# Kernel optimization log

Measured on AMD Instinct MI355X. Metric: run time of the kernel, lower is better.

## Reference

```python
import jax, jax.numpy as jnp
import numpy as np

ROUTINGS = 3

def _squash_size1(s):
    # Faithful to squash(tensor, dim=-1) applied on a size-1 last dim:
    # squared_norm degenerates to elementwise s**2.
    sq = s * s
    return (sq / (1.0 + sq)) * s / jnp.sqrt(sq + 1e-9)

def setup_inputs() -> dict:
    key = jax.random.key(0)
    k1, k2 = jax.random.split(key)
    B, I, Din = 16, 1152, 16
    N, D = 32, 64
    inputs = jax.random.normal(k1, (B, I, Din), dtype=jnp.float32)
    W = jax.random.normal(k2, (1, N, I, D, Din), dtype=jnp.float32)
    return {"inputs": inputs, "W": W}

def reference(inputs, W):
    # inputs: [B, I, Din]; W: [1, N, I, D, Din]
    # torch: matmul(W, inputs.unsqueeze(1).unsqueeze(4)) -> [B,N,I,D,1]; drop trailing 1.
    x_hat = jnp.einsum('nidk,bik->bnid', W[0], inputs)  # [B, N, I, D]
    b = jnp.zeros_like(x_hat)                            # [B, N, I, D] (quirk: carries D axis)
    outputs = None
    for i in range(ROUTINGS):
        c = jax.nn.softmax(b, axis=2)                    # softmax over input capsules
        s = jnp.sum(c * x_hat, axis=2)                   # [B, N, D]
        outputs = _squash_size1(s)                       # elementwise squash (size-1 dim quirk)
        if i < ROUTINGS - 1:
            # (inputs_hat * outputs).sum(dim=-1) over size-1 dim == elementwise product
            b = b + x_hat * outputs[:, :, None, :]
    return outputs[..., None]                            # [B, N, D, 1] (after squeeze(2))
```

## Files before the change

### kernel.cpp

```cpp
#include <hip/hip_runtime.h>
#include <hip/hip_bf16.h>
#include <math.h>

#define B_   16
#define N_   32
#define I_   1152
#define DIN  16
#define D_   64
#define TI   8
#define IB   (I_/TI)
#define IC   16
#define BND  (B_*N_*D_)

#if __has_builtin(__builtin_amdgcn_exp2f)
#define EXP2(x) __builtin_amdgcn_exp2f(x)
#else
#define EXP2(x) exp2f(x)
#endif

#define LOG2E 1.4426950408889634f

typedef __attribute__((ext_vector_type(8))) short short8v;
typedef __attribute__((ext_vector_type(4))) float f32x4;
typedef __attribute__((ext_vector_type(4))) unsigned int u32x4;
typedef __attribute__((ext_vector_type(2))) unsigned int u32x2;

__device__ __forceinline__ float squash1(float s) {
    float sq = s * s;
    return (sq / (1.0f + sq)) * s * rsqrtf(sq + 1e-9f);
}
__device__ __forceinline__ unsigned short bfh(float v) {
    return __builtin_bit_cast(unsigned short, __float2bfloat16(v));
}
__device__ __forceinline__ float bff(unsigned short u) {
    unsigned int x = ((unsigned int)u) << 16;
    return __builtin_bit_cast(float, x);
}

__global__ __launch_bounds__(256, 4) void k_xhat(const float* __restrict__ inp,
                                                 const float* __restrict__ W,
                                                 unsigned short* __restrict__ xh2,
                                                 float* __restrict__ part) {
    __shared__ __align__(16) unsigned short xs[2048];
    const int bx = blockIdx.x;
    const int n  = bx / IB;
    const int ib = bx % IB;
    const int i0 = ib * TI;
    const int t  = threadIdx.x;
    const int l  = t & 63;
    const int mt = t >> 6;
    const int row = l & 15;
    const int ko  = (l >> 4) & 1;

    {
        const int sb  = t >> 4;
        const int sil = (t >> 1) & 7;
        const int sko = t & 1;
        const float* src = inp + (size_t)sb * (I_ * DIN) + (size_t)(i0 + sil) * DIN + sko * 8;
        f32x4 a0 = *(const f32x4*)src;
        f32x4 a1 = *(const f32x4*)(src + 4);
        u32x4 p;
        p.x = ((unsigned)bfh(a0.y) << 16) | bfh(a0.x);
        p.y = ((unsigned)bfh(a0.w) << 16) | bfh(a0.z);
        p.z = ((unsigned)bfh(a1.y) << 16) | bfh(a1.x);
        p.w = ((unsigned)bfh(a1.w) << 16) | bfh(a1.z);
        int base = (sb * 256 + sil * 32 + sko * 16) ^ ((sb & 7) << 4);
        *(u32x4*)((char*)xs + base) = p;
    }
    __syncthreads();

    const float* wb = W + ((size_t)(n * I_ + i0) * 64 + mt * 16 + row) * 16 + ko * 8;
    f32x4 wv[16];
    #pragma unroll
    for (int i = 0; i < 8; ++i) {
        const f32x4* p = (const f32x4*)(wb + (size_t)i * 1024);
        wv[2 * i] = p[0]; wv[2 * i + 1] = p[1];
    }

    f32x4 acc[TI];
    #pragma unroll
    for (int i = 0; i < TI; ++i) acc[i] = (f32x4){0.f, 0.f, 0.f, 0.f};

    const bool loHalf = (l >= 32);
    #pragma unroll
    for (int i = 0; i < TI; ++i) {
        int xaddr = ((l & 15) * 256 + i * 32 + ko * 16) ^ (((l & 15) & 7) << 4);
        short8v bfrag = *(const short8v*)((const char*)xs + xaddr);
        short8v afrag;
        #pragma unroll
        for (int j = 0; j < 8; ++j) {
            float w = wv[2 * i + (j >> 2)][j & 3];
            unsigned short hi = bfh(w);
            unsigned short lo = bfh(w - bff(hi));
            afrag[j] = (short)(loHalf ? lo : hi);
        }
        acc[i] = __builtin_amdgcn_mfma_f32_16x16x32_bf16(afrag, bfrag, acc[i], 0, 0, 0);
    }

    f32x4 s0v = acc[0];
    #pragma unroll
    for (int i = 1; i < TI; ++i) s0v += acc[i];
    size_t pidx = (((size_t)ib * B_ + (l & 15)) * N_ + n) * 64 + mt * 16 + (l >> 4) * 4;
    *(f32x4*)(part + pidx) = s0v;

    #pragma unroll
    for (int i = 0; i < TI; ++i) {
        u32x2 v;
        v.x = ((unsigned)bfh(acc[i][1]) << 16) | bfh(acc[i][0]);
        v.y = ((unsigned)bfh(acc[i][3]) << 16) | bfh(acc[i][2]);
        size_t off = (size_t)(n * I_ + i0 + i) * 1024 + (size_t)t * 4;
        *reinterpret_cast<u32x2*>(xh2 + off) = v;
    }
}

__global__ __launch_bounds__(256) void k_out0(const float* __restrict__ part,
                                              float* __restrict__ coef) {
    const int t = blockIdx.x * 256 + threadIdx.x;
    float s = 0.0f;
    for (int j = 0; j < IB; ++j) s += part[(size_t)j * BND + t];
    s *= (1.0f / (float)I_);
    coef[t] = squash1(s);
}

__global__ __launch_bounds__(256) void k_rpart(const unsigned short* __restrict__ xh2,
                                               const float* __restrict__ coef,
                                               float* __restrict__ part2) {
    const int bx = blockIdx.x;
    const int n  = bx >> 4;
    const int ic = bx & 15;
    const int t  = threadIdx.x;
    const int b  = t & 15;
    const int d0 = (t >> 4) * 4;

    const unsigned short* base = xh2 + ((size_t)n * I_ + (size_t)ic * (I_ / IC)) * 1024
                               + (size_t)t * 4;
    f32x4 c4 = *(const f32x4*)(coef + ((size_t)b * N_ + n) * 64 + d0);
    float c2[4] = {c4.x * LOG2E, c4.y * LOG2E, c4.z * LOG2E, c4.w * LOG2E};
    float z[4] = {0, 0, 0, 0}, a[4] = {0, 0, 0, 0};

    #pragma unroll 8
    for (int i = 0; i < I_ / IC; ++i) {
        u32x2 u = *(const u32x2*)(base + (size_t)i * 1024);
        unsigned short s4[4] = {(unsigned short)(u.x & 0xffffu), (unsigned short)(u.x >> 16),
                                (unsigned short)(u.y & 0xffffu), (unsigned short)(u.y >> 16)};
        #pragma unroll
        for (int j = 0; j < 4; ++j) {
            float x = bff(s4[j]);
            float e = EXP2(x * c2[j]);
            z[j] += e;
            a[j] = fmaf(e, x, a[j]);
        }
    }

    size_t pidx = ((((size_t)ic * N_ + n) * 16 + b) * 64 + d0) * 2;
    f32x4 v0 = {z[0], a[0], z[1], a[1]};
    f32x4 v1 = {z[2], a[2], z[3], a[3]};
    *(f32x4*)(part2 + pidx)     = v0;
    *(f32x4*)(part2 + pidx + 4) = v1;
}

__global__ __launch_bounds__(256) void k_rfin(const float* __restrict__ part2,
                                              const float* __restrict__ coefIn,
                                              float* __restrict__ outp,
                                              int final_) {
    const int gid = blockIdx.x * 256 + threadIdx.x;
    float Z = 0.0f, A = 0.0f;
    #pragma unroll
    for (int ic = 0; ic < IC; ++ic) {
        const float* p = part2 + ((size_t)ic * BND + gid) * 2;
        Z += p[0];
        A += p[1];
    }
    const int d = gid & 63, b = (gid >> 6) & 15, n = gid >> 10;
    const int ci = (b * N_ + n) * D_ + d;
    float o = squash1(A / Z);
    outp[ci] = final_ ? o : (coefIn[ci] + o);
}

extern "C" void kernel_launch(void* const* d_in, const int* in_sizes, int n_in,
                              void* d_out, int out_size, void* d_ws, size_t ws_size,
                              hipStream_t stream) {
    const float* inp = (const float*)d_in[0];
    const float* W   = (const float*)d_in[1];
    float* out = (float*)d_out;

    unsigned short* xh2 = (unsigned short*)d_ws;
    float* part  = (float*)((char*)d_ws + 75497472);
    float* part2 = (float*)((char*)d_ws + 94371840);
    float* coef  = (float*)((char*)d_ws + 98566144);

    k_xhat<<<dim3(N_ * IB), dim3(256), 0, stream>>>(inp, W, xh2, part);
    k_out0<<<dim3(BND / 256), dim3(256), 0, stream>>>(part, coef);
    k_rpart<<<dim3(N_ * IC), dim3(256), 0, stream>>>(xh2, coef, part2);
    k_rfin <<<dim3(BND / 256), dim3(256), 0, stream>>>(part2, coef, coef, 0);
    k_rpart<<<dim3(N_ * IC), dim3(256), 0, stream>>>(xh2, coef, part2);
    k_rfin <<<dim3(BND / 256), dim3(256), 0, stream>>>(part2, coef, out, 1);
}
```

Baseline: 80.87 us.

## Double TI per block and software-pipeline W loads in xhat kernel

Each block of the x_hat kernel now covers 16 input capsules instead of 8, which halves the number of blocks and the size of the partial-sum buffer read by k_out0. W is loaded in groups of four capsules into two alternating register buffers so that the next group's global loads overlap the bf16 split and MFMA work on the current group. Results are packed to bf16 right after each MFMA instead of being held in accumulators. The changes raise register and LDS use, so launch bounds drop to 3 blocks per SM, which may reduce occupancy.

```diff
diff --git a/kernel.cpp b/kernel.cpp
--- a/kernel.cpp
+++ b/kernel.cpp
@@ -7,7 +7,7 @@
 #define I_   1152
 #define DIN  16
 #define D_   64
-#define TI   8
+#define TI   16
 #define IB   (I_/TI)
 #define IC   16
 #define BND  (B_*N_*D_)
@@ -29,19 +29,18 @@
     float sq = s * s;
     return (sq / (1.0f + sq)) * s * rsqrtf(sq + 1e-9f);
 }
-__device__ __forceinline__ unsigned short bfh(float v) {
-    return __builtin_bit_cast(unsigned short, __float2bfloat16(v));
-}
-__device__ __forceinline__ float bff(unsigned short u) {
-    unsigned int x = ((unsigned int)u) << 16;
-    return __builtin_bit_cast(float, x);
-}
-
-__global__ __launch_bounds__(256, 4) void k_xhat(const float* __restrict__ inp,
+__device__ __forceinline__ unsigned int bfh(float v) {
+    return (unsigned int)__builtin_bit_cast(unsigned short, __float2bfloat16(v));
+}
+__device__ __forceinline__ float bff(unsigned int hi16) {
+    return __builtin_bit_cast(float, hi16 << 16);
+}
+
+__global__ __launch_bounds__(256, 3) void k_xhat(const float* __restrict__ inp,
                                                  const float* __restrict__ W,
                                                  unsigned short* __restrict__ xh2,
                                                  float* __restrict__ part) {
-    __shared__ __align__(16) unsigned short xs[2048];
+    __shared__ __align__(16) unsigned short xs[4096];
     const int bx = blockIdx.x;
     const int n  = bx / IB;
     const int ib = bx % IB;
@@ -51,63 +50,80 @@
     const int mt = t >> 6;
     const int row = l & 15;
     const int ko  = (l >> 4) & 1;
-
-    {
-        const int sb  = t >> 4;
-        const int sil = (t >> 1) & 7;
-        const int sko = t & 1;
-        const float* src = inp + (size_t)sb * (I_ * DIN) + (size_t)(i0 + sil) * DIN + sko * 8;
+    const bool loHalf = (l >= 32);
+
+    #pragma unroll
+    for (int rep = 0; rep < 2; ++rep) {
+        int s   = rep * 256 + t;
+        int bb  = s >> 5;
+        int il  = (s >> 1) & 15;
+        int sko = s & 1;
+        const float* src = inp + (size_t)bb * (I_ * DIN) + (size_t)(i0 + il) * DIN + sko * 8;
         f32x4 a0 = *(const f32x4*)src;
         f32x4 a1 = *(const f32x4*)(src + 4);
         u32x4 p;
-        p.x = ((unsigned)bfh(a0.y) << 16) | bfh(a0.x);
-        p.y = ((unsigned)bfh(a0.w) << 16) | bfh(a0.z);
-        p.z = ((unsigned)bfh(a1.y) << 16) | bfh(a1.x);
-        p.w = ((unsigned)bfh(a1.w) << 16) | bfh(a1.z);
-        int base = (sb * 256 + sil * 32 + sko * 16) ^ ((sb & 7) << 4);
+        p.x = (bfh(a0.y) << 16) | bfh(a0.x);
+        p.y = (bfh(a0.w) << 16) | bfh(a0.z);
+        p.z = (bfh(a1.y) << 16) | bfh(a1.x);
+        p.w = (bfh(a1.w) << 16) | bfh(a1.z);
+        int base = (bb * 512 + il * 32 + sko * 16) ^ ((bb & 7) << 4);
         *(u32x4*)((char*)xs + base) = p;
     }
     __syncthreads();
 
     const float* wb = W + ((size_t)(n * I_ + i0) * 64 + mt * 16 + row) * 16 + ko * 8;
-    f32x4 wv[16];
-    #pragma unroll
-    for (int i = 0; i < 8; ++i) {
-        const f32x4* p = (const f32x4*)(wb + (size_t)i * 1024);
-        wv[2 * i] = p[0]; wv[2 * i + 1] = p[1];
-    }
-
-    f32x4 acc[TI];
-    #pragma unroll
-    for (int i = 0; i < TI; ++i) acc[i] = (f32x4){0.f, 0.f, 0.f, 0.f};
-
-    const bool loHalf = (l >= 32);
-    #pragma unroll
-    for (int i = 0; i < TI; ++i) {
-        int xaddr = ((l & 15) * 256 + i * 32 + ko * 16) ^ (((l & 15) & 7) << 4);
-        short8v bfrag = *(const short8v*)((const char*)xs + xaddr);
-        short8v afrag;
-        #pragma unroll
-        for (int j = 0; j < 8; ++j) {
-            float w = wv[2 * i + (j >> 2)][j & 3];
-            unsigned short hi = bfh(w);
-            unsigned short lo = bfh(w - bff(hi));
-            afrag[j] = (short)(loHalf ? lo : hi);
-        }
-        acc[i] = __builtin_amdgcn_mfma_f32_16x16x32_bf16(afrag, bfrag, acc[i], 0, 0, 0);
-    }
-
-    f32x4 s0v = acc[0];
-    #pragma unroll
-    for (int i = 1; i < TI; ++i) s0v += acc[i];
+
+    unsigned int pk[TI * 2];
+    f32x4 s0v = {0.f, 0.f, 0.f, 0.f};
+
+#define LOADG(DST, C) {                                                        \
+        _Pragma("unroll")                                                      \
+        for (int j = 0; j < 4; ++j) {                                          \
+            const f32x4* p = (const f32x4*)(wb + (size_t)((C) * 4 + j) * 1024);\
+            DST[2 * j] = p[0]; DST[2 * j + 1] = p[1];                          \
+        } }
+
+#define COMPG(SRC, C) {                                                        \
+        _Pragma("unroll")                                                      \
+        for (int j = 0; j < 4; ++j) {                                          \
+            const int i = (C) * 4 + j;                                         \
+            int xaddr = ((l & 15) * 512 + i * 32 + ko * 16) ^ (((l & 15) & 7) << 4); \
+            short8v bfrag = *(const short8v*)((const char*)xs + xaddr);        \
+            short8v afrag;                                                     \
+            _Pragma("unroll")                                                  \
+            for (int q = 0; q < 8; ++q) {                                      \
+                float wq = SRC[2 * j + (q >> 2)][q & 3];                       \
+                unsigned int hi = bfh(wq);                                     \
+                unsigned int lo = bfh(wq - bff(hi));                           \
+                afrag[q] = (short)(loHalf ? lo : hi);                          \
+            }                                                                  \
+            f32x4 acc = __builtin_amdgcn_mfma_f32_16x16x32_bf16(               \
+                afrag, bfrag, (f32x4){0.f, 0.f, 0.f, 0.f}, 0, 0, 0);           \
+            s0v += acc;                                                        \
+            pk[i * 2]     = (bfh(acc[1]) << 16) | bfh(acc[0]);                 \
+            pk[i * 2 + 1] = (bfh(acc[3]) << 16) | bfh(acc[2]);                 \
+        } }
+
+    f32x4 wA[8], wB[8];
+    LOADG(wA, 0)
+    LOADG(wB, 1)
+    COMPG(wA, 0)
+    LOADG(wA, 2)
+    COMPG(wB, 1)
+    LOADG(wB, 3)
+    COMPG(wA, 2)
+    COMPG(wB, 3)
+#undef LOADG
+#undef COMPG
+
     size_t pidx = (((size_t)ib * B_ + (l & 15)) * N_ + n) * 64 + mt * 16 + (l >> 4) * 4;
     *(f32x4*)(part + pidx) = s0v;
 
     #pragma unroll
     for (int i = 0; i < TI; ++i) {
         u32x2 v;
-        v.x = ((unsigned)bfh(acc[i][1]) << 16) | bfh(acc[i][0]);
-        v.y = ((unsigned)bfh(acc[i][3]) << 16) | bfh(acc[i][2]);
+        v.x = pk[i * 2];
+        v.y = pk[i * 2 + 1];
         size_t off = (size_t)(n * I_ + i0 + i) * 1024 + (size_t)t * 4;
         *reinterpret_cast<u32x2*>(xh2 + off) = v;
     }
@@ -186,8 +202,8 @@
 
     unsigned short* xh2 = (unsigned short*)d_ws;
     float* part  = (float*)((char*)d_ws + 75497472);
-    float* part2 = (float*)((char*)d_ws + 94371840);
-    float* coef  = (float*)((char*)d_ws + 98566144);
+    float* part2 = (float*)((char*)d_ws + 84934656);
+    float* coef  = (float*)((char*)d_ws + 89128960);
 
     k_xhat<<<dim3(N_ * IB), dim3(256), 0, stream>>>(inp, W, xh2, part);
     k_out0<<<dim3(BND / 256), dim3(256), 0, stream>>>(part, coef);
```

Result: faster. 76.63 us (-5.2%).
